# Kernel optimization log

Hardware: AMD Instinct MI355X
Metric: run time of the kernel (lower is better)

The kernel has to match this reference:

```python
import jax, jax.numpy as jnp
import numpy as np

NUM_LINKS = 4096
BUDGET = 100.0      # total_power_budget
PMAX = 0.1          # per_link_max
N_BISECT = 60       # bisection iterations (fp32 converges well before this)


def setup_inputs() -> dict:
    key = jax.random.key(0)
    raw_power = jax.random.normal(key, (8192, NUM_LINKS), dtype=jnp.float32)
    return {"raw_power": raw_power}


def _project(raw):
    """Euclidean projection of each row of raw onto {p : 0<=p<=PMAX, sum(p)<=BUDGET}.

    Closed-form water-filling: if clip(raw,0,PMAX) is feasible it is the answer;
    otherwise p = clip(raw - tau, 0, PMAX) with tau chosen so sum(p) = BUDGET
    (found by batched bisection + one implicit-function Newton correction,
    which also gives the exact QP-projection Jacobian).
    """
    clipped = jnp.clip(raw, 0.0, PMAX)
    feasible = jnp.sum(clipped, axis=-1, keepdims=True) <= BUDGET  # (B,1)

    raw_sg = jax.lax.stop_gradient(raw)
    lo = jnp.min(raw_sg, axis=-1, keepdims=True) - PMAX  # g(lo) = n*PMAX >= BUDGET
    hi = jnp.max(raw_sg, axis=-1, keepdims=True)         # g(hi) = 0

    def body(_, lohi):
        lo, hi = lohi
        mid = 0.5 * (lo + hi)
        g = jnp.sum(jnp.clip(raw_sg - mid, 0.0, PMAX), axis=-1, keepdims=True)
        too_big = g > BUDGET  # tau must increase
        return (jnp.where(too_big, mid, lo), jnp.where(too_big, hi, mid))

    lo, hi = jax.lax.fori_loop(0, N_BISECT, body, (lo, hi))
    tau0 = 0.5 * (lo + hi)  # (B,1), no gradient

    # Implicit-function (Newton) correction: g(tau) = sum(clip(raw-tau,0,PMAX)) = BUDGET.
    # dg/dtau = -n_active, dg/draw_i = active_i  => dtau/draw_i = active_i / n_active.
    active = (raw_sg - tau0 > 0.0) & (raw_sg - tau0 < PMAX)
    n_active = jnp.maximum(jnp.sum(active, axis=-1, keepdims=True).astype(raw.dtype), 1.0)
    g0 = jnp.sum(jnp.clip(raw - tau0, 0.0, PMAX), axis=-1, keepdims=True)
    tau = tau0 + (g0 - BUDGET) / n_active  # value ~= tau0, correct gradient

    p_budget = jnp.clip(raw - tau, 0.0, PMAX)
    return jnp.where(feasible, clipped, p_budget)


def reference(raw_power) -> jnp.ndarray:
    return _project(raw_power)
```

## Files before the change

### kernel.cpp

```cpp
#include <hip/hip_runtime.h>

#define NLINKS 4096
#define VEC 16

typedef float fvec4 __attribute__((ext_vector_type(4)));

constexpr float kPmax = 0.1f;
constexpr float kBudget = 100.0f;
constexpr int kGrid = 8;
constexpr int kFallbackIters = 8;

__device__ __forceinline__ float clip01(float x) {
  return __builtin_amdgcn_fmed3f(x, 0.0f, kPmax);
}

template <int N>
__device__ __forceinline__ void waveReduceSumN(float* x) {
#pragma unroll
  for (int m = 32; m >= 1; m >>= 1) {
    float t[N];
#pragma unroll
    for (int k = 0; k < N; ++k) t[k] = __shfl_xor(x[k], m, 64);
#pragma unroll
    for (int k = 0; k < N; ++k) x[k] += t[k];
  }
}
__device__ __forceinline__ float waveReduceMax(float x) {
#pragma unroll
  for (int m = 32; m >= 1; m >>= 1) x = fmaxf(x, __shfl_xor(x, m, 64));
  return x;
}

__global__ __launch_bounds__(256, 2) void proj_kernel(
    const float* __restrict__ raw, float* __restrict__ out, int rows) {
  const int wave = threadIdx.x >> 6;
  const int lane = threadIdx.x & 63;
  const int row = blockIdx.x * 4 + wave;
  if (row >= rows) return;

  const fvec4* rp = (const fvec4*)(raw + (size_t)row * NLINKS);
  fvec4* op = (fvec4*)(out + (size_t)row * NLINKS);

  fvec4 v[VEC];
#pragma unroll
  for (int j = 0; j < VEC; ++j) v[j] = __builtin_nontemporal_load(&rp[lane + 64 * j]);

  const float pts[kGrid] = {0.45f, 0.52f, 0.58f, 0.62f, 0.66f, 0.70f, 0.78f, 0.90f};

  float mx = -1e30f;
  float s[kGrid + 1];
#pragma unroll
  for (int k = 0; k <= kGrid; ++k) s[k] = 0.f;
#pragma unroll
  for (int j = 0; j < VEC; ++j) {
#pragma unroll
    for (int c = 0; c < 4; ++c) {
      const float x = v[j][c];
      mx = fmaxf(mx, x);
      s[0] += clip01(x);
#pragma unroll
      for (int i = 0; i < kGrid; ++i) s[i + 1] += clip01(x - pts[i]);
    }
  }
  waveReduceSumN<kGrid + 1>(s);
  mx = waveReduceMax(mx);
  const float fs = s[0];

  if (fs <= kBudget) {
#pragma unroll
    for (int j = 0; j < VEC; ++j) {
      fvec4 o;
#pragma unroll
      for (int c = 0; c < 4; ++c) o[c] = clip01(v[j][c]);
      __builtin_nontemporal_store(o, &op[lane + 64 * j]);
    }
    return;
  }

  float a = 0.f, ga = fs, b = mx, gb = 0.f;
  bool need_iter = true;
  if (s[1] < kBudget) {
    a = 0.f; ga = fs; b = pts[0]; gb = s[1];
  } else if (s[kGrid] > kBudget) {
    a = pts[kGrid - 1]; ga = s[kGrid]; b = mx; gb = 0.f;
  } else {
#pragma unroll
    for (int i = 0; i < kGrid - 1; ++i) {
      if (s[i + 1] >= kBudget && s[i + 2] <= kBudget) {
        a = pts[i]; ga = s[i + 1]; b = pts[i + 1]; gb = s[i + 2];
        need_iter = false;
        break;
      }
    }
  }

  if (need_iter) {
    int side = 0;
#pragma unroll 1
    for (int it = 0; it < kFallbackIters; ++it) {
      const float denom = gb - ga;
      float t = (denom != 0.f) ? b - (gb - kBudget) * (b - a) / denom
                               : 0.5f * (a + b);
      if (!(t > a && t < b)) t = 0.5f * (a + b);
      float s0 = 0.f, s1 = 0.f, s2 = 0.f, s3 = 0.f;
#pragma unroll
      for (int j = 0; j < VEC; ++j) {
        s0 += clip01(v[j].x - t);
        s1 += clip01(v[j].y - t);
        s2 += clip01(v[j].z - t);
        s3 += clip01(v[j].w - t);
      }
      float g = (s0 + s1) + (s2 + s3);
      waveReduceSumN<1>(&g);
      if (g > kBudget) {
        a = t; ga = g;
        if (side == 1) gb = kBudget + 0.5f * (gb - kBudget);
        side = 1;
      } else {
        b = t; gb = g;
        if (side == -1) ga = kBudget + 0.5f * (ga - kBudget);
        side = -1;
      }
    }
  }

  const float dd = ga - gb;
  float tau0 = (dd != 0.f) ? a + (ga - kBudget) * (b - a) / dd : 0.5f * (a + b);
  if (!(tau0 >= a && tau0 <= b)) tau0 = 0.5f * (a + b);

  float gn[2] = {0.f, 0.f};
#pragma unroll
  for (int j = 0; j < VEC; ++j) {
#pragma unroll
    for (int c = 0; c < 4; ++c) {
      const float t = v[j][c] - tau0;
      gn[0] += clip01(t);
      gn[1] += (t > 0.f && t < kPmax) ? 1.f : 0.f;
    }
  }
  waveReduceSumN<2>(gn);
  const float tau = tau0 + (gn[0] - kBudget) / fmaxf(gn[1], 1.0f);

#pragma unroll
  for (int j = 0; j < VEC; ++j) {
    fvec4 o;
#pragma unroll
    for (int c = 0; c < 4; ++c) o[c] = clip01(v[j][c] - tau);
    __builtin_nontemporal_store(o, &op[lane + 64 * j]);
  }
}

extern "C" void kernel_launch(void* const* d_in, const int* in_sizes, int n_in,
                              void* d_out, int out_size, void* d_ws, size_t ws_size,
                              hipStream_t stream) {
  const float* raw = (const float*)d_in[0];
  float* out = (float*)d_out;
  const int rows = in_sizes[0] / NLINKS;
  const int blocks = (rows + 3) / 4;
  hipLaunchKernelGGL(proj_kernel, dim3(blocks), dim3(256), 0, stream,
                     raw, out, rows);
}
```

Before: 226.8 us.

## Stream row from memory per pass instead of holding it in registers

Drops the 64-float-per-lane register cache of the row and instead re-reads it from global memory in each pass, using a 4-deep rolling prefetch buffer. Compiler barriers keep the loads from being hoisted and merged across passes, and the launch-bounds occupancy hint is removed. The aim is lower register pressure so more waves run per CU and hide latency better. The cost is that each row is read from memory (or cache) 3 or more times instead of once, which adds bandwidth pressure on a kernel that is likely memory-bound.

```diff
diff --git a/kernel.cpp b/kernel.cpp
--- a/kernel.cpp
+++ b/kernel.cpp
@@ -31,7 +31,22 @@
   return x;
 }
 
-__global__ __launch_bounds__(256, 2) void proj_kernel(
+
+template <typename F>
+__device__ __forceinline__ void streamRow(const fvec4* __restrict__ rp,
+                                          int lane, F&& f) {
+  fvec4 buf[4];
+#pragma unroll
+  for (int j = 0; j < 4; ++j) buf[j] = rp[lane + 64 * j];
+#pragma unroll
+  for (int j = 0; j < VEC; ++j) {
+    const fvec4 x4 = buf[j & 3];
+    if (j + 4 < VEC) buf[j & 3] = rp[lane + 64 * (j + 4)];
+    f(x4, j);
+  }
+}
+
+__global__ __launch_bounds__(256) void proj_kernel(
     const float* __restrict__ raw, float* __restrict__ out, int rows) {
   const int wave = threadIdx.x >> 6;
   const int lane = threadIdx.x & 63;
@@ -41,39 +56,35 @@
   const fvec4* rp = (const fvec4*)(raw + (size_t)row * NLINKS);
   fvec4* op = (fvec4*)(out + (size_t)row * NLINKS);
 
-  fvec4 v[VEC];
-#pragma unroll
-  for (int j = 0; j < VEC; ++j) v[j] = __builtin_nontemporal_load(&rp[lane + 64 * j]);
-
   const float pts[kGrid] = {0.45f, 0.52f, 0.58f, 0.62f, 0.66f, 0.70f, 0.78f, 0.90f};
 
   float mx = -1e30f;
   float s[kGrid + 1];
 #pragma unroll
   for (int k = 0; k <= kGrid; ++k) s[k] = 0.f;
-#pragma unroll
-  for (int j = 0; j < VEC; ++j) {
+  streamRow(rp, lane, [&](const fvec4& x4, int j) {
 #pragma unroll
     for (int c = 0; c < 4; ++c) {
-      const float x = v[j][c];
+      const float x = x4[c];
       mx = fmaxf(mx, x);
       s[0] += clip01(x);
 #pragma unroll
       for (int i = 0; i < kGrid; ++i) s[i + 1] += clip01(x - pts[i]);
     }
-  }
+  });
   waveReduceSumN<kGrid + 1>(s);
   mx = waveReduceMax(mx);
   const float fs = s[0];
 
+  asm volatile("" ::: "memory");
+
   if (fs <= kBudget) {
-#pragma unroll
-    for (int j = 0; j < VEC; ++j) {
+    streamRow(rp, lane, [&](const fvec4& x4, int j) {
       fvec4 o;
 #pragma unroll
-      for (int c = 0; c < 4; ++c) o[c] = clip01(v[j][c]);
+      for (int c = 0; c < 4; ++c) o[c] = clip01(x4[c]);
       __builtin_nontemporal_store(o, &op[lane + 64 * j]);
-    }
+    });
     return;
   }
 
@@ -103,13 +114,12 @@
                                : 0.5f * (a + b);
       if (!(t > a && t < b)) t = 0.5f * (a + b);
       float s0 = 0.f, s1 = 0.f, s2 = 0.f, s3 = 0.f;
-#pragma unroll
-      for (int j = 0; j < VEC; ++j) {
-        s0 += clip01(v[j].x - t);
-        s1 += clip01(v[j].y - t);
-        s2 += clip01(v[j].z - t);
-        s3 += clip01(v[j].w - t);
-      }
+      streamRow(rp, lane, [&](const fvec4& x4, int j) {
+        s0 += clip01(x4.x - t);
+        s1 += clip01(x4.y - t);
+        s2 += clip01(x4.z - t);
+        s3 += clip01(x4.w - t);
+      });
       float g = (s0 + s1) + (s2 + s3);
       waveReduceSumN<1>(&g);
       if (g > kBudget) {
@@ -121,6 +131,7 @@
         if (side == -1) ga = kBudget + 0.5f * (ga - kBudget);
         side = -1;
       }
+      asm volatile("" ::: "memory");
     }
   }
 
@@ -129,25 +140,25 @@
   if (!(tau0 >= a && tau0 <= b)) tau0 = 0.5f * (a + b);
 
   float gn[2] = {0.f, 0.f};
-#pragma unroll
-  for (int j = 0; j < VEC; ++j) {
+  streamRow(rp, lane, [&](const fvec4& x4, int j) {
 #pragma unroll
     for (int c = 0; c < 4; ++c) {
-      const float t = v[j][c] - tau0;
+      const float t = x4[c] - tau0;
       gn[0] += clip01(t);
       gn[1] += (t > 0.f && t < kPmax) ? 1.f : 0.f;
     }
-  }
+  });
   waveReduceSumN<2>(gn);
   const float tau = tau0 + (gn[0] - kBudget) / fmaxf(gn[1], 1.0f);
 
-#pragma unroll
-  for (int j = 0; j < VEC; ++j) {
+  asm volatile("" ::: "memory");
+
+  streamRow(rp, lane, [&](const fvec4& x4, int j) {
     fvec4 o;
 #pragma unroll
-    for (int c = 0; c < 4; ++c) o[c] = clip01(v[j][c] - tau);
+    for (int c = 0; c < 4; ++c) o[c] = clip01(x4[c] - tau);
     __builtin_nontemporal_store(o, &op[lane + 64 * j]);
-  }
+  });
 }
 
 extern "C" void kernel_launch(void* const* d_in, const int* in_sizes, int n_in,
```

New measurement: 243.6 us. 1.07x slower.

## Process each row with a full 256-thread block instead of one wave

Applied to the files above, without the earlier changes.

Each row is now split across four waves in one block, with cross-wave reductions done through LDS and __syncthreads, instead of one wave handling a whole row. Each thread holds 4 vec4 registers rather than 16, which frees registers and allows higher occupancy; the launch bound hint changes accordingly. The cost is extra block-level barriers and LDS traffic on every reduction, including inside the fallback iteration loop.

```diff
diff --git a/kernel.cpp b/kernel.cpp
--- a/kernel.cpp
+++ b/kernel.cpp
@@ -1,7 +1,7 @@
 #include <hip/hip_runtime.h>
 
 #define NLINKS 4096
-#define VEC 16
+#define CHUNKS 4
 
 typedef float fvec4 __attribute__((ext_vector_type(4)));
 
@@ -31,19 +31,25 @@
   return x;
 }
 
-__global__ __launch_bounds__(256, 2) void proj_kernel(
+__global__ __launch_bounds__(256) void proj_kernel(
     const float* __restrict__ raw, float* __restrict__ out, int rows) {
-  const int wave = threadIdx.x >> 6;
-  const int lane = threadIdx.x & 63;
-  const int row = blockIdx.x * 4 + wave;
+  const int row = blockIdx.x;
   if (row >= rows) return;
+  const int tid = threadIdx.x;
+  const int wave = tid >> 6;
+  const int lane = tid & 63;
+
+  __shared__ float ldsA[4][12];
+  __shared__ float ldsF[4];
+  __shared__ float ldsN[4][2];
 
   const fvec4* rp = (const fvec4*)(raw + (size_t)row * NLINKS);
   fvec4* op = (fvec4*)(out + (size_t)row * NLINKS);
 
-  fvec4 v[VEC];
+  fvec4 v[CHUNKS];
 #pragma unroll
-  for (int j = 0; j < VEC; ++j) v[j] = __builtin_nontemporal_load(&rp[lane + 64 * j]);
+  for (int j = 0; j < CHUNKS; ++j)
+    v[j] = __builtin_nontemporal_load(&rp[tid + 256 * j]);
 
   const float pts[kGrid] = {0.45f, 0.52f, 0.58f, 0.62f, 0.66f, 0.70f, 0.78f, 0.90f};
 
@@ -52,7 +58,7 @@
 #pragma unroll
   for (int k = 0; k <= kGrid; ++k) s[k] = 0.f;
 #pragma unroll
-  for (int j = 0; j < VEC; ++j) {
+  for (int j = 0; j < CHUNKS; ++j) {
 #pragma unroll
     for (int c = 0; c < 4; ++c) {
       const float x = v[j][c];
@@ -64,15 +70,26 @@
   }
   waveReduceSumN<kGrid + 1>(s);
   mx = waveReduceMax(mx);
+  if (lane == 0) {
+#pragma unroll
+    for (int k = 0; k <= kGrid; ++k) ldsA[wave][k] = s[k];
+    ldsA[wave][kGrid + 1] = mx;
+  }
+  __syncthreads();
+#pragma unroll
+  for (int k = 0; k <= kGrid; ++k)
+    s[k] = (ldsA[0][k] + ldsA[1][k]) + (ldsA[2][k] + ldsA[3][k]);
+  mx = fmaxf(fmaxf(ldsA[0][kGrid + 1], ldsA[1][kGrid + 1]),
+             fmaxf(ldsA[2][kGrid + 1], ldsA[3][kGrid + 1]));
   const float fs = s[0];
 
   if (fs <= kBudget) {
 #pragma unroll
-    for (int j = 0; j < VEC; ++j) {
+    for (int j = 0; j < CHUNKS; ++j) {
       fvec4 o;
 #pragma unroll
       for (int c = 0; c < 4; ++c) o[c] = clip01(v[j][c]);
-      __builtin_nontemporal_store(o, &op[lane + 64 * j]);
+      __builtin_nontemporal_store(o, &op[tid + 256 * j]);
     }
     return;
   }
@@ -104,7 +121,7 @@
       if (!(t > a && t < b)) t = 0.5f * (a + b);
       float s0 = 0.f, s1 = 0.f, s2 = 0.f, s3 = 0.f;
 #pragma unroll
-      for (int j = 0; j < VEC; ++j) {
+      for (int j = 0; j < CHUNKS; ++j) {
         s0 += clip01(v[j].x - t);
         s1 += clip01(v[j].y - t);
         s2 += clip01(v[j].z - t);
@@ -112,6 +129,10 @@
       }
       float g = (s0 + s1) + (s2 + s3);
       waveReduceSumN<1>(&g);
+      if (lane == 0) ldsF[wave] = g;
+      __syncthreads();
+      g = (ldsF[0] + ldsF[1]) + (ldsF[2] + ldsF[3]);
+      __syncthreads();
       if (g > kBudget) {
         a = t; ga = g;
         if (side == 1) gb = kBudget + 0.5f * (gb - kBudget);
@@ -130,7 +151,7 @@
 
   float gn[2] = {0.f, 0.f};
 #pragma unroll
-  for (int j = 0; j < VEC; ++j) {
+  for (int j = 0; j < CHUNKS; ++j) {
 #pragma unroll
     for (int c = 0; c < 4; ++c) {
       const float t = v[j][c] - tau0;
@@ -139,14 +160,21 @@
     }
   }
   waveReduceSumN<2>(gn);
+  if (lane == 0) {
+    ldsN[wave][0] = gn[0];
+    ldsN[wave][1] = gn[1];
+  }
+  __syncthreads();
+  gn[0] = (ldsN[0][0] + ldsN[1][0]) + (ldsN[2][0] + ldsN[3][0]);
+  gn[1] = (ldsN[0][1] + ldsN[1][1]) + (ldsN[2][1] + ldsN[3][1]);
   const float tau = tau0 + (gn[0] - kBudget) / fmaxf(gn[1], 1.0f);
 
 #pragma unroll
-  for (int j = 0; j < VEC; ++j) {
+  for (int j = 0; j < CHUNKS; ++j) {
     fvec4 o;
 #pragma unroll
     for (int c = 0; c < 4; ++c) o[c] = clip01(v[j][c] - tau);
-    __builtin_nontemporal_store(o, &op[lane + 64 * j]);
+    __builtin_nontemporal_store(o, &op[tid + 256 * j]);
   }
 }
 
@@ -156,7 +184,6 @@
   const float* raw = (const float*)d_in[0];
   float* out = (float*)d_out;
   const int rows = in_sizes[0] / NLINKS;
-  const int blocks = (rows + 3) / 4;
-  hipLaunchKernelGGL(proj_kernel, dim3(blocks), dim3(256), 0, stream,
+  hipLaunchKernelGGL(proj_kernel, dim3(rows), dim3(256), 0, stream,
                      raw, out, rows);
 }
```

Result: faster. 221.4 us (-2.3%).
